# Performance work log

Hardware: AMD Instinct MI355X
Metric: run time of the kernel (lower is better)

Reference implementation:

```python
import jax, jax.numpy as jnp
import numpy as np

D_MODEL = 1024
NHEAD = 16
HEAD_DIM = D_MODEL // NHEAD


def setup_inputs() -> dict:
    key = jax.random.key(0)
    ks = jax.random.split(key, 9)
    s = 0.02
    x = jax.random.normal(ks[0], (2, 2048, D_MODEL), dtype=jnp.float32)
    Wq = jax.random.normal(ks[1], (D_MODEL, D_MODEL), dtype=jnp.float32) * s
    bq = jnp.zeros((D_MODEL,), jnp.float32)
    Wk = jax.random.normal(ks[2], (D_MODEL, D_MODEL), dtype=jnp.float32) * s
    bk = jnp.zeros((D_MODEL,), jnp.float32)
    Wv = jax.random.normal(ks[3], (D_MODEL, D_MODEL), dtype=jnp.float32) * s
    bv = jnp.zeros((D_MODEL,), jnp.float32)
    Wo = jax.random.normal(ks[4], (D_MODEL, D_MODEL), dtype=jnp.float32) * s
    bo = jnp.zeros((D_MODEL,), jnp.float32)
    return {"x": x, "Wq": Wq, "bq": bq, "Wk": Wk, "bk": bk,
            "Wv": Wv, "bv": bv, "Wo": Wo, "bo": bo}


def _rope(x, sin, cos):
    # x: [B, L, H, Dh]; rotate-half as in the torch module
    half = x.shape[-1] // 2
    x1, x2 = x[..., :half], x[..., half:]
    rotated = jnp.concatenate([-x2, x1], axis=-1)
    return x * cos + rotated * sin


def reference(x, Wq, bq, Wk, bk, Wv, bv, Wo, bo):
    B, L, D = x.shape
    H, Dh = NHEAD, HEAD_DIM
    q = (x @ Wq.T + bq).reshape(B, L, H, Dh)
    k = (x @ Wk.T + bk).reshape(B, L, H, Dh)
    v = (x @ Wv.T + bv).reshape(B, L, H, Dh)

    inv_freq = 1.0 / (10000.0 ** (jnp.arange(0, Dh, 2, dtype=jnp.float32) / Dh))
    t = jnp.arange(L, dtype=jnp.float32)
    freqs = jnp.einsum('i,j->ij', t, inv_freq)          # [L, Dh/2]
    emb = jnp.concatenate([freqs, freqs], axis=-1)      # [L, Dh]
    cos = jnp.cos(emb)[None, :, None, :]
    sin = jnp.sin(emb)[None, :, None, :]

    q = _rope(q, sin, cos)
    k = _rope(k, sin, cos)

    # [B, H, L, L]
    scores = jnp.einsum('bqhd,bkhd->bhqk', q, k) / jnp.sqrt(jnp.float32(Dh))
    attn = jax.nn.softmax(scores, axis=-1)
    # dropout in eval mode = identity (p given as 0.0)
    out = jnp.einsum('bhqk,bkhd->bqhd', attn, v).reshape(B, L, D)
    return out @ Wo.T + bo
```

## Files before the change

kernel.cpp:

```cpp
#include <hip/hip_runtime.h>
#include <math.h>

#define D_MODEL 1024
#define NHEAD 16
#define HEAD_DIM 64
#define L_SEQ 2048
#define BATCH 2
#define M_ROWS 4096
#define SC_Q 0.18033688011112042f

typedef __attribute__((ext_vector_type(8))) short short8;
typedef __attribute__((ext_vector_type(4))) float floatx4;
typedef __attribute__((ext_vector_type(2))) __fp16 half2_t;
typedef __attribute__((ext_vector_type(4))) __fp16 half4_t;
typedef __attribute__((ext_vector_type(8))) __fp16 half8_t;

#if __has_builtin(__builtin_amdgcn_exp2f)
#define EXP2F(x) __builtin_amdgcn_exp2f(x)
#else
#define EXP2F(x) exp2f(x)
#endif

__device__ inline unsigned f2bf_u(float x) {
    unsigned u = __float_as_uint(x);
    return (u + 0x7fffu + ((u >> 16) & 1u)) >> 16;
}

__device__ inline void gl_lds16(const void* g, void* l) {
    __builtin_amdgcn_global_load_lds((const __attribute__((address_space(1))) void*)g,
                                     (__attribute__((address_space(3))) void*)l, 16, 0, 0);
}

__device__ inline void permlane16_swap(unsigned& a, unsigned& b) {
#if __has_builtin(__builtin_amdgcn_permlane16_swap)
    auto r = __builtin_amdgcn_permlane16_swap(a, b, false, false);
    a = r[0];
    b = r[1];
#else
    asm("v_permlane16_swap_b32 %0, %1" : "+v"(a), "+v"(b));
#endif
}

__global__ __launch_bounds__(256) void cvt_all(
    const float* __restrict__ x,  const float* __restrict__ wq,
    const float* __restrict__ wk, const float* __restrict__ wv,
    const float* __restrict__ wo,
    unsigned short* __restrict__ xb,  unsigned short* __restrict__ wqb,
    unsigned short* __restrict__ wkb, unsigned short* __restrict__ wvb,
    unsigned short* __restrict__ wob, float* __restrict__ rt) {
    if (blockIdx.y == 5) {
        for (int idx = blockIdx.x * 256 + threadIdx.x; idx < L_SEQ * 16;
             idx += gridDim.x * 256) {
            int l = idx >> 4, f = idx & 15;
            float if0 = (float)pow(10000.0, -(double)f / 32.0);
            float if1 = (float)pow(10000.0, -(double)(f + 16) / 32.0);
            float s0, c0, s1, c1;
            sincosf((float)l * if0, &s0, &c0);
            sincosf((float)l * if1, &s1, &c1);
            float4 v = {c0, c1, s0, s1};
            *(float4*)(rt + (size_t)idx * 4) = v;
        }
        return;
    }
    const float* s; unsigned short* d; int n;
    switch (blockIdx.y) {
        case 0:  s = x;  d = xb;  n = M_ROWS * D_MODEL; break;
        case 1:  s = wq; d = wqb; n = D_MODEL * D_MODEL; break;
        case 2:  s = wk; d = wkb; n = D_MODEL * D_MODEL; break;
        case 3:  s = wv; d = wvb; n = D_MODEL * D_MODEL; break;
        default: s = wo; d = wob; n = D_MODEL * D_MODEL; break;
    }
    int stride = gridDim.x * 256 * 4;
    for (int i = (blockIdx.x * 256 + threadIdx.x) * 4; i < n; i += stride) {
        float4 v = *(const float4*)(s + i);
        ushort4 o;
        o.x = (unsigned short)f2bf_u(v.x);
        o.y = (unsigned short)f2bf_u(v.y);
        o.z = (unsigned short)f2bf_u(v.z);
        o.w = (unsigned short)f2bf_u(v.w);
        *(ushort4*)(d + i) = o;
    }
}

__global__ __launch_bounds__(256) void gemm_qkv(
    const unsigned short* __restrict__ xb,
    const unsigned short* __restrict__ wqb, const unsigned short* __restrict__ wkb,
    const unsigned short* __restrict__ wvb,
    const float* __restrict__ bq, const float* __restrict__ bk,
    const float* __restrict__ bv, const float* __restrict__ rt,
    unsigned short* __restrict__ qo, unsigned short* __restrict__ ko,
    unsigned short* __restrict__ vo) {
    __shared__ __align__(16) unsigned short As[128 * 32];
    __shared__ __align__(16) unsigned short Bs[128 * 32];

    const int K = D_MODEL;
    const int tid = threadIdx.x;
    const int lane = tid & 63;
    const int w = tid >> 6;
    const int wm = (w & 1) * 64;
    const int wn = (w >> 1) * 64;
    const int m0 = blockIdx.x * 128;
    const int n0 = blockIdx.y * 128;

    const unsigned short* Wsel; const float* bsel;
    unsigned short* osel; int mode; float oscale;
    if (blockIdx.z == 0)      { Wsel = wqb; bsel = bq; osel = qo; mode = 1; oscale = SC_Q; }
    else if (blockIdx.z == 1) { Wsel = wkb; bsel = bk; osel = ko; mode = 1; oscale = 1.0f; }
    else                      { Wsel = wvb; bsel = bv; osel = vo; mode = 2; oscale = 1.0f; }

    floatx4 acc[4][4];
#pragma unroll
    for (int i = 0; i < 4; ++i)
#pragma unroll
        for (int j = 0; j < 4; ++j) acc[i][j] = (floatx4){0.f, 0.f, 0.f, 0.f};

    const int sr = lane >> 2;
    const int ss = lane & 3;
    const unsigned short* Ag = xb + (size_t)m0 * K;
    const unsigned short* Bg = Wsel + (size_t)n0 * K;

    for (int k0 = 0; k0 < K; k0 += 32) {
        __syncthreads();
#pragma unroll
        for (int t = 0; t < 2; ++t) {
            int R0 = t * 64 + w * 16;
            int r = R0 + sr;
            int c = ss ^ ((r >> 1) & 3);
            gl_lds16(Ag + (size_t)r * K + k0 + c * 8, (void*)(As + R0 * 32));
            gl_lds16(Bg + (size_t)r * K + k0 + c * 8, (void*)(Bs + R0 * 32));
        }
        __syncthreads();

        short8 af[4], bf[4];
#pragma unroll
        for (int mt = 0; mt < 4; ++mt) {
            int ar = wm + mt * 16 + (lane & 15);
            int slot = (lane >> 4) ^ ((ar >> 1) & 3);
            af[mt] = *(const short8*)(As + ar * 32 + slot * 8);
        }
#pragma unroll
        for (int nt = 0; nt < 4; ++nt) {
            int br = wn + nt * 16 + (lane & 15);
            int slot = (lane >> 4) ^ ((br >> 1) & 3);
            bf[nt] = *(const short8*)(Bs + br * 32 + slot * 8);
        }
#pragma unroll
        for (int mt = 0; mt < 4; ++mt)
#pragma unroll
            for (int nt = 0; nt < 4; ++nt)
                acc[mt][nt] = __builtin_amdgcn_mfma_f32_16x16x32_bf16(
                    af[mt], bf[nt], acc[mt][nt], 0, 0, 0);
    }

#pragma unroll
    for (int nt = 0; nt < 4; ++nt) {
        float bn = bsel[n0 + wn + nt * 16 + (lane & 15)];
#pragma unroll
        for (int mt = 0; mt < 4; ++mt)
#pragma unroll
            for (int i = 0; i < 4; ++i) acc[mt][nt][i] += bn;
    }

    const int h = (n0 + wn) >> 6;

    if (mode == 1) {
#pragma unroll
        for (int mt = 0; mt < 4; ++mt)
#pragma unroll
            for (int i = 0; i < 4; ++i) {
                int m = m0 + wm + mt * 16 + (lane >> 4) * 4 + i;
                int b = m >> 11, l = m & (L_SEQ - 1);
                float4 tc = *(const float4*)(rt + ((size_t)(l * 16 + (lane & 15)) << 2));
#pragma unroll
                for (int nt = 0; nt < 4; ++nt) {
                    int dh = nt * 16 + (lane & 15);
                    float partner = acc[mt][nt ^ 2][i];
                    float rot = (nt < 2) ? -partner : partner;
                    float c = (nt & 1) ? tc.y : tc.x;
                    float s = (nt & 1) ? tc.w : tc.z;
                    float val = (acc[mt][nt][i] * c + rot * s) * oscale;
                    size_t idx = (((size_t)(b * NHEAD + h)) * L_SEQ + l) * HEAD_DIM + dh;
                    osel[idx] = (unsigned short)f2bf_u(val);
                }
            }
    } else {
#pragma unroll
        for (int mt = 0; mt < 4; ++mt)
#pragma unroll
            for (int ih = 0; ih < 4; ih += 2) {
                int m = m0 + wm + mt * 16 + (lane >> 4) * 4 + ih;
                int b = m >> 11, l = m & (L_SEQ - 1);
#pragma unroll
                for (int nt = 0; nt < 4; ++nt) {
                    int dh = nt * 16 + (lane & 15);
                    union { half2_t h; unsigned u; } cv;
                    cv.h = __builtin_amdgcn_cvt_pkrtz(acc[mt][nt][ih], acc[mt][nt][ih + 1]);
                    size_t idx = (((size_t)(b * NHEAD + h)) * HEAD_DIM + dh) * L_SEQ + l;
                    *(unsigned*)(vo + idx) = cv.u;
                }
            }
    }
}

__global__ __launch_bounds__(256) void gemm_out(
    const unsigned short* __restrict__ A, const unsigned short* __restrict__ Wb,
    const float* __restrict__ bias, float* __restrict__ out) {
    __shared__ __align__(16) unsigned short As[64 * 32];
    __shared__ __align__(16) unsigned short Bs[128 * 32];

    const int K = D_MODEL;
    const int tid = threadIdx.x;
    const int lane = tid & 63;
    const int w = tid >> 6;
    const int wm = (w & 1) * 32;
    const int wn = (w >> 1) * 64;
    const int m0 = blockIdx.x * 64;
    const int n0 = blockIdx.y * 128;

    floatx4 acc[2][4];
#pragma unroll
    for (int i = 0; i < 2; ++i)
#pragma unroll
        for (int j = 0; j < 4; ++j) acc[i][j] = (floatx4){0.f, 0.f, 0.f, 0.f};

    const int sr = lane >> 2;
    const int ss = lane & 3;
    const unsigned short* Ag = A + (size_t)m0 * K;
    const unsigned short* Bg = Wb + (size_t)n0 * K;

    for (int k0 = 0; k0 < K; k0 += 32) {
        __syncthreads();
        {
            int r = w * 16 + sr;
            int c = ss ^ ((r >> 1) & 3);
            gl_lds16(Ag + (size_t)r * K + k0 + c * 8, (void*)(As + (w * 16) * 32));
        }
#pragma unroll
        for (int t = 0; t < 2; ++t) {
            int R0 = t * 64 + w * 16;
            int r = R0 + sr;
            int c = ss ^ ((r >> 1) & 3);
            gl_lds16(Bg + (size_t)r * K + k0 + c * 8, (void*)(Bs + R0 * 32));
        }
        __syncthreads();

        short8 af[2], bf[4];
#pragma unroll
        for (int mt = 0; mt < 2; ++mt) {
            int ar = wm + mt * 16 + (lane & 15);
            int slot = (lane >> 4) ^ ((ar >> 1) & 3);
            af[mt] = *(const short8*)(As + ar * 32 + slot * 8);
        }
#pragma unroll
        for (int nt = 0; nt < 4; ++nt) {
            int br = wn + nt * 16 + (lane & 15);
            int slot = (lane >> 4) ^ ((br >> 1) & 3);
            bf[nt] = *(const short8*)(Bs + br * 32 + slot * 8);
        }
#pragma unroll
        for (int mt = 0; mt < 2; ++mt)
#pragma unroll
            for (int nt = 0; nt < 4; ++nt)
                acc[mt][nt] = __builtin_amdgcn_mfma_f32_16x16x32_bf16(
                    af[mt], bf[nt], acc[mt][nt], 0, 0, 0);
    }

#pragma unroll
    for (int nt = 0; nt < 4; ++nt) {
        int n = n0 + wn + nt * 16 + (lane & 15);
        float bn = bias[n];
#pragma unroll
        for (int mt = 0; mt < 2; ++mt)
#pragma unroll
            for (int i = 0; i < 4; ++i) {
                int m = m0 + wm + mt * 16 + (lane >> 4) * 4 + i;
                out[(size_t)m * D_MODEL + n] = acc[mt][nt][i] + bn;
            }
    }
}

template <int NZ>
__global__ __launch_bounds__(256, 4) void attn_mfma(
    const unsigned short* __restrict__ q, const unsigned short* __restrict__ k,
    const unsigned short* __restrict__ vt,
    float* __restrict__ opart, float* __restrict__ lpart,
    unsigned short* __restrict__ ao) {
    __shared__ __align__(16) unsigned short Ks[128 * 64];
    __shared__ __align__(16) unsigned short Vs[64 * 128];

    const int tid = threadIdx.x;
    const int lane = tid & 63;
    const int w = tid >> 6;
    const int quad = lane >> 4;
    const int ln = lane & 15;
    const int bh = blockIdx.y;
    const int q0 = blockIdx.x * 128;
    const int z = blockIdx.z;
    const int kvbase = z * (L_SEQ / NZ);

    const unsigned short* qb = q + (size_t)bh * L_SEQ * HEAD_DIM;
    const unsigned short* kb = k + (size_t)bh * L_SEQ * HEAD_DIM;
    const unsigned short* vb = vt + (size_t)bh * HEAD_DIM * L_SEQ;

    short8 qf[2][2];
#pragma unroll
    for (int ntq = 0; ntq < 2; ++ntq)
#pragma unroll
        for (int ks = 0; ks < 2; ++ks)
            qf[ntq][ks] = *(const short8*)(
                qb + (size_t)(q0 + w * 32 + ntq * 16 + ln) * HEAD_DIM
                + ks * 32 + quad * 8);

    floatx4 o[2][4];
    floatx4 ls[2];
#pragma unroll
    for (int ntq = 0; ntq < 2; ++ntq) {
        ls[ntq] = (floatx4){0.f, 0.f, 0.f, 0.f};
#pragma unroll
        for (int j = 0; j < 4; ++j) o[ntq][j] = (floatx4){0.f, 0.f, 0.f, 0.f};
    }

    half8_t ones8;
#pragma unroll
    for (int j = 0; j < 8; ++j) ones8[j] = (__fp16)1.0f;

    const int srk = lane >> 3;
    const int ssk = lane & 7;
    const int srv = lane >> 4;
    const int ssv = lane & 15;
    const int pb = ((quad & 1) << 1) | (quad >> 1);

    for (int t = 0; t < L_SEQ / (128 * NZ); ++t) {
        int kv0 = kvbase + t * 128;
        __syncthreads();
#pragma unroll
        for (int tt = 0; tt < 4; ++tt) {
            {
                int R0 = tt * 32 + w * 8;
                int r = R0 + srk;
                int c = ssk ^ (r & 7);
                gl_lds16(kb + (size_t)(kv0 + r) * HEAD_DIM + c * 8, (void*)(Ks + R0 * 64));
            }
            {
                int R0 = tt * 16 + w * 4;
                int r = R0 + srv;
                int c = ssv ^ (r & 15);
                gl_lds16(vb + (size_t)r * L_SEQ + kv0 + c * 8, (void*)(Vs + R0 * 128));
            }
        }
        __syncthreads();

#pragma unroll
        for (int mt2 = 0; mt2 < 4; ++mt2) {
            floatx4 s[2][2];
#pragma unroll
            for (int c = 0; c < 2; ++c) {
                int ar = mt2 * 32 + c * 16 + ln;
                short8 kf0 = *(const short8*)(Ks + ar * 64 + ((quad) ^ (ar & 7)) * 8);
                short8 kf1 = *(const short8*)(Ks + ar * 64 + ((4 + quad) ^ (ar & 7)) * 8);

                floatx4 t0 = (floatx4){0.f, 0.f, 0.f, 0.f};
                floatx4 t1 = (floatx4){0.f, 0.f, 0.f, 0.f};
                t0 = __builtin_amdgcn_mfma_f32_16x16x32_bf16(kf0, qf[0][0], t0, 0, 0, 0);
                t0 = __builtin_amdgcn_mfma_f32_16x16x32_bf16(kf1, qf[0][1], t0, 0, 0, 0);
                t1 = __builtin_amdgcn_mfma_f32_16x16x32_bf16(kf0, qf[1][0], t1, 0, 0, 0);
                t1 = __builtin_amdgcn_mfma_f32_16x16x32_bf16(kf1, qf[1][1], t1, 0, 0, 0);
                s[c][0] = t0;
                s[c][1] = t1;
            }

            half8_t vf[4];
#pragma unroll
            for (int ntd = 0; ntd < 4; ++ntd) {
                int row = ntd * 16 + ln;
                int slot = (mt2 * 4 + pb) ^ (row & 15);
                vf[ntd] = *(const half8_t*)(Vs + row * 128 + slot * 8);
            }

#pragma unroll
            for (int tq = 0; tq < 2; ++tq) {
                union { half2_t h; unsigned u; } c0l, c0h, c1l, c1h;
                c0l.h = __builtin_amdgcn_cvt_pkrtz(EXP2F(s[0][tq][0]), EXP2F(s[0][tq][1]));
                c0h.h = __builtin_amdgcn_cvt_pkrtz(EXP2F(s[0][tq][2]), EXP2F(s[0][tq][3]));
                c1l.h = __builtin_amdgcn_cvt_pkrtz(EXP2F(s[1][tq][0]), EXP2F(s[1][tq][1]));
                c1h.h = __builtin_amdgcn_cvt_pkrtz(EXP2F(s[1][tq][2]), EXP2F(s[1][tq][3]));
                unsigned a0 = c0l.u, b0 = c1l.u;
                unsigned a1 = c0h.u, b1 = c1h.u;
                permlane16_swap(a0, b0);
                permlane16_swap(a1, b1);
                union { half8_t h8; unsigned u[4]; } af;
                af.u[0] = a0; af.u[1] = a1; af.u[2] = b0; af.u[3] = b1;

                ls[tq] = __builtin_amdgcn_mfma_f32_16x16x32_f16(af.h8, ones8, ls[tq], 0, 0, 0);
#pragma unroll
                for (int ntd = 0; ntd < 4; ++ntd)
                    o[tq][ntd] = __builtin_amdgcn_mfma_f32_16x16x32_f16(
                        af.h8, vf[ntd], o[tq][ntd], 0, 0, 0);
            }
        }
    }

    if (NZ == 1) {
        const int b = bh >> 4, h = bh & (NHEAD - 1);
#pragma unroll
        for (int ntq = 0; ntq < 2; ++ntq)
#pragma unroll
            for (int i = 0; i < 4; ++i) {
                int l = q0 + w * 32 + ntq * 16 + quad * 4 + i;
                float inv = 1.0f / ls[ntq][i];
#pragma unroll
                for (int ntd = 0; ntd < 4; ++ntd) {
                    int dh = ntd * 16 + ln;
                    size_t idx = ((size_t)b * L_SEQ + l) * D_MODEL + h * HEAD_DIM + dh;
                    ao[idx] = (unsigned short)f2bf_u(o[ntq][ntd][i] * inv);
                }
            }
    } else {
        const size_t base = ((size_t)z * (BATCH * NHEAD) + bh) * L_SEQ;
#pragma unroll
        for (int ntq = 0; ntq < 2; ++ntq)
#pragma unroll
            for (int i = 0; i < 4; ++i) {
                int l = q0 + w * 32 + ntq * 16 + quad * 4 + i;
#pragma unroll
                for (int ntd = 0; ntd < 4; ++ntd) {
                    int dh = ntd * 16 + ln;
                    opart[(base + l) * HEAD_DIM + dh] = o[ntq][ntd][i];
                }
            }
        if (ln == 0) {
#pragma unroll
            for (int ntq = 0; ntq < 2; ++ntq)
#pragma unroll
                for (int i = 0; i < 4; ++i) {
                    int l = q0 + w * 32 + ntq * 16 + quad * 4 + i;
                    lpart[base + l] = ls[ntq][i];
                }
        }
    }
}

__global__ __launch_bounds__(256) void attn_combine(
    const float* __restrict__ opart, const float* __restrict__ lpart,
    unsigned short* __restrict__ ao) {
    const size_t R = (size_t)BATCH * NHEAD * L_SEQ;
    int e = blockIdx.x * 256 + threadIdx.x;
    int r = e >> 4;
    int dh0 = (e & 15) * 4;
    float4 a = *(const float4*)(opart + (size_t)r * HEAD_DIM + dh0);
    float4 c = *(const float4*)(opart + (R + r) * HEAD_DIM + dh0);
    float inv = 1.0f / (lpart[r] + lpart[R + r]);
    int bh = r >> 11, l = r & (L_SEQ - 1);
    int b = bh >> 4, h = bh & (NHEAD - 1);
    ushort4 ov;
    ov.x = (unsigned short)f2bf_u((a.x + c.x) * inv);
    ov.y = (unsigned short)f2bf_u((a.y + c.y) * inv);
    ov.z = (unsigned short)f2bf_u((a.z + c.z) * inv);
    ov.w = (unsigned short)f2bf_u((a.w + c.w) * inv);
    *(ushort4*)(ao + ((size_t)b * L_SEQ + l) * D_MODEL + h * HEAD_DIM + dh0) = ov;
}

extern "C" void kernel_launch(void* const* d_in, const int* in_sizes, int n_in,
                              void* d_out, int out_size, void* d_ws, size_t ws_size,
                              hipStream_t stream) {
    const float* x  = (const float*)d_in[0];
    const float* Wq = (const float*)d_in[1];
    const float* bq = (const float*)d_in[2];
    const float* Wk = (const float*)d_in[3];
    const float* bk = (const float*)d_in[4];
    const float* Wv = (const float*)d_in[5];
    const float* bv = (const float*)d_in[6];
    const float* Wo = (const float*)d_in[7];
    const float* bo = (const float*)d_in[8];
    float* outp = (float*)d_out;

    const size_t XE = (size_t)M_ROWS * D_MODEL;
    const size_t WE = (size_t)D_MODEL * D_MODEL;
    unsigned short* wqb = (unsigned short*)d_ws;
    unsigned short* wkb = wqb + WE;
    unsigned short* wvb = wkb + WE;
    unsigned short* wob = wvb + WE;
    unsigned short* qbf = wob + WE;
    unsigned short* kbf = qbf + XE;
    unsigned short* vtb = kbf + XE;
    unsigned short* xb  = vtb + XE;
    unsigned short* aob = xb;
    float* rt    = (float*)(xb + XE);
    float* lpart = rt;
    float* opart = rt + 131072;

    const size_t base_bytes  = (4 * WE + 4 * XE) * 2 + 131072 * 4;
    const size_t split_bytes = base_bytes + (size_t)8 * 1024 * 1024 * 4;
    const bool use_split = ws_size >= split_bytes;

    cvt_all<<<dim3(1024, 6), 256, 0, stream>>>(x, Wq, Wk, Wv, Wo,
                                               xb, wqb, wkb, wvb, wob, rt);

    gemm_qkv<<<dim3(M_ROWS / 128, D_MODEL / 128, 3), 256, 0, stream>>>(
        xb, wqb, wkb, wvb, bq, bk, bv, rt, qbf, kbf, vtb);

    if (use_split) {
        attn_mfma<2><<<dim3(L_SEQ / 128, BATCH * NHEAD, 2), 256, 0, stream>>>(
            qbf, kbf, vtb, opart, lpart, nullptr);
        attn_combine<<<dim3(4096), 256, 0, stream>>>(opart, lpart, aob);
    } else {
        attn_mfma<1><<<dim3(L_SEQ / 128, BATCH * NHEAD, 1), 256, 0, stream>>>(
            qbf, kbf, vtb, nullptr, nullptr, aob);
    }

    gemm_out<<<dim3(M_ROWS / 64, D_MODEL / 128), 256, 0, stream>>>(aob, wob, bo, outp);
}
```

Before: 197.5 us.

## Double-buffer K/V LDS tiles and remap workgroup order in attention kernel

Attention kernel now uses two LDS buffers for K and V tiles. It issues the next tile's global-to-LDS loads before computing on the current tile, so load latency overlaps with MFMA work and one barrier per iteration goes away. It also remaps the linear workgroup index with a stride-8 interleave, presumably to spread neighbouring blocks across XCDs for cache locality. LDS use doubles to 64KB per block, which may reduce occupancy under launch_bounds(256,4).

```diff
diff --git a/kernel.cpp b/kernel.cpp
--- a/kernel.cpp
+++ b/kernel.cpp
@@ -285,17 +285,23 @@
     const unsigned short* __restrict__ vt,
     float* __restrict__ opart, float* __restrict__ lpart,
     unsigned short* __restrict__ ao) {
-    __shared__ __align__(16) unsigned short Ks[128 * 64];
-    __shared__ __align__(16) unsigned short Vs[64 * 128];
+    __shared__ __align__(16) unsigned short Ks[2][128 * 64];
+    __shared__ __align__(16) unsigned short Vs[2][64 * 128];
 
     const int tid = threadIdx.x;
     const int lane = tid & 63;
     const int w = tid >> 6;
     const int quad = lane >> 4;
     const int ln = lane & 15;
-    const int bh = blockIdx.y;
-    const int q0 = blockIdx.x * 128;
-    const int z = blockIdx.z;
+
+    const int GX = L_SEQ / 128;
+    const int nwg = GX * BATCH * NHEAD * NZ;
+    int lin = (blockIdx.z * (BATCH * NHEAD) + blockIdx.y) * GX + blockIdx.x;
+    lin = (lin & 7) * (nwg >> 3) + (lin >> 3);
+    const int q0 = (lin & (GX - 1)) * 128;
+    const int rest = lin >> 4;
+    const int bh = rest & (BATCH * NHEAD - 1);
+    const int z = rest >> 5;
     const int kvbase = z * (L_SEQ / NZ);
 
     const unsigned short* qb = q + (size_t)bh * L_SEQ * HEAD_DIM;
@@ -330,34 +336,35 @@
     const int ssv = lane & 15;
     const int pb = ((quad & 1) << 1) | (quad >> 1);
 
-    for (int t = 0; t < L_SEQ / (128 * NZ); ++t) {
-        int kv0 = kvbase + t * 128;
-        __syncthreads();
+    auto stage_tile = [&](int buf, int kv0) {
 #pragma unroll
         for (int tt = 0; tt < 4; ++tt) {
             {
                 int R0 = tt * 32 + w * 8;
                 int r = R0 + srk;
                 int c = ssk ^ (r & 7);
-                gl_lds16(kb + (size_t)(kv0 + r) * HEAD_DIM + c * 8, (void*)(Ks + R0 * 64));
+                gl_lds16(kb + (size_t)(kv0 + r) * HEAD_DIM + c * 8,
+                         (void*)(Ks[buf] + R0 * 64));
             }
             {
                 int R0 = tt * 16 + w * 4;
                 int r = R0 + srv;
                 int c = ssv ^ (r & 15);
-                gl_lds16(vb + (size_t)r * L_SEQ + kv0 + c * 8, (void*)(Vs + R0 * 128));
-            }
-        }
-        __syncthreads();
-
+                gl_lds16(vb + (size_t)r * L_SEQ + kv0 + c * 8,
+                         (void*)(Vs[buf] + R0 * 128));
+            }
+        }
+    };
+
+    auto compute_tile = [&](const unsigned short* KsP, const unsigned short* VsP) {
 #pragma unroll
         for (int mt2 = 0; mt2 < 4; ++mt2) {
             floatx4 s[2][2];
 #pragma unroll
             for (int c = 0; c < 2; ++c) {
                 int ar = mt2 * 32 + c * 16 + ln;
-                short8 kf0 = *(const short8*)(Ks + ar * 64 + ((quad) ^ (ar & 7)) * 8);
-                short8 kf1 = *(const short8*)(Ks + ar * 64 + ((4 + quad) ^ (ar & 7)) * 8);
+                short8 kf0 = *(const short8*)(KsP + ar * 64 + ((quad) ^ (ar & 7)) * 8);
+                short8 kf1 = *(const short8*)(KsP + ar * 64 + ((4 + quad) ^ (ar & 7)) * 8);
 
                 floatx4 t0 = (floatx4){0.f, 0.f, 0.f, 0.f};
                 floatx4 t1 = (floatx4){0.f, 0.f, 0.f, 0.f};
@@ -374,7 +381,7 @@
             for (int ntd = 0; ntd < 4; ++ntd) {
                 int row = ntd * 16 + ln;
                 int slot = (mt2 * 4 + pb) ^ (row & 15);
-                vf[ntd] = *(const half8_t*)(Vs + row * 128 + slot * 8);
+                vf[ntd] = *(const half8_t*)(VsP + row * 128 + slot * 8);
             }
 
 #pragma unroll
@@ -397,6 +404,21 @@
                     o[tq][ntd] = __builtin_amdgcn_mfma_f32_16x16x32_f16(
                         af.h8, vf[ntd], o[tq][ntd], 0, 0, 0);
             }
+        }
+    };
+
+    const int NT = L_SEQ / (128 * NZ);
+    stage_tile(0, kvbase);
+    __syncthreads();
+    int cur = 0;
+    for (int t = 0; t < NT; ++t) {
+        if (t + 1 < NT) {
+            stage_tile(cur ^ 1, kvbase + (t + 1) * 128);
+            compute_tile(Ks[cur], Vs[cur]);
+            __syncthreads();
+            cur ^= 1;
+        } else {
+            compute_tile(Ks[cur], Vs[cur]);
         }
     }
 
```

After: 196.8 us. About the same (-0.4%).

## Drop split-KV attention and remap blocks so XCDs share heads

Applied to the files above, without the earlier changes.

Removes the two-way KV split and its combine kernel, so each attention block now processes the full sequence and writes normalized bf16 output directly. It also remaps the linear block index so that consecutive hardware-dispatched blocks (round-robin across the 8 XCDs) land on the same head's query tiles, improving K/V reuse in each XCD's L2. This removes the partial-output write/read traffic and one launch, but halves the grid to 512 blocks, which lowers parallelism and may leave CUs underused.

```diff
diff --git a/kernel.cpp b/kernel.cpp
--- a/kernel.cpp
+++ b/kernel.cpp
@@ -279,11 +279,9 @@
     }
 }
 
-template <int NZ>
 __global__ __launch_bounds__(256, 4) void attn_mfma(
     const unsigned short* __restrict__ q, const unsigned short* __restrict__ k,
     const unsigned short* __restrict__ vt,
-    float* __restrict__ opart, float* __restrict__ lpart,
     unsigned short* __restrict__ ao) {
     __shared__ __align__(16) unsigned short Ks[128 * 64];
     __shared__ __align__(16) unsigned short Vs[64 * 128];
@@ -293,10 +291,12 @@
     const int w = tid >> 6;
     const int quad = lane >> 4;
     const int ln = lane & 15;
-    const int bh = blockIdx.y;
-    const int q0 = blockIdx.x * 128;
-    const int z = blockIdx.z;
-    const int kvbase = z * (L_SEQ / NZ);
+
+    const int GX = L_SEQ / 128;
+    int lin = blockIdx.y * GX + blockIdx.x;
+    lin = (lin & 7) * 64 + (lin >> 3);
+    const int q0 = (lin & (GX - 1)) * 128;
+    const int bh = lin >> 4;
 
     const unsigned short* qb = q + (size_t)bh * L_SEQ * HEAD_DIM;
     const unsigned short* kb = k + (size_t)bh * L_SEQ * HEAD_DIM;
@@ -330,8 +330,8 @@
     const int ssv = lane & 15;
     const int pb = ((quad & 1) << 1) | (quad >> 1);
 
-    for (int t = 0; t < L_SEQ / (128 * NZ); ++t) {
-        int kv0 = kvbase + t * 128;
+    for (int t = 0; t < L_SEQ / 128; ++t) {
+        int kv0 = t * 128;
         __syncthreads();
 #pragma unroll
         for (int tt = 0; tt < 4; ++tt) {
@@ -400,64 +400,20 @@
         }
     }
 
-    if (NZ == 1) {
-        const int b = bh >> 4, h = bh & (NHEAD - 1);
-#pragma unroll
-        for (int ntq = 0; ntq < 2; ++ntq)
-#pragma unroll
-            for (int i = 0; i < 4; ++i) {
-                int l = q0 + w * 32 + ntq * 16 + quad * 4 + i;
-                float inv = 1.0f / ls[ntq][i];
-#pragma unroll
-                for (int ntd = 0; ntd < 4; ++ntd) {
-                    int dh = ntd * 16 + ln;
-                    size_t idx = ((size_t)b * L_SEQ + l) * D_MODEL + h * HEAD_DIM + dh;
-                    ao[idx] = (unsigned short)f2bf_u(o[ntq][ntd][i] * inv);
-                }
-            }
-    } else {
-        const size_t base = ((size_t)z * (BATCH * NHEAD) + bh) * L_SEQ;
-#pragma unroll
-        for (int ntq = 0; ntq < 2; ++ntq)
-#pragma unroll
-            for (int i = 0; i < 4; ++i) {
-                int l = q0 + w * 32 + ntq * 16 + quad * 4 + i;
-#pragma unroll
-                for (int ntd = 0; ntd < 4; ++ntd) {
-                    int dh = ntd * 16 + ln;
-                    opart[(base + l) * HEAD_DIM + dh] = o[ntq][ntd][i];
-                }
-            }
-        if (ln == 0) {
-#pragma unroll
-            for (int ntq = 0; ntq < 2; ++ntq)
-#pragma unroll
-                for (int i = 0; i < 4; ++i) {
-                    int l = q0 + w * 32 + ntq * 16 + quad * 4 + i;
-                    lpart[base + l] = ls[ntq][i];
-                }
-        }
-    }
-}
-
-__global__ __launch_bounds__(256) void attn_combine(
-    const float* __restrict__ opart, const float* __restrict__ lpart,
-    unsigned short* __restrict__ ao) {
-    const size_t R = (size_t)BATCH * NHEAD * L_SEQ;
-    int e = blockIdx.x * 256 + threadIdx.x;
-    int r = e >> 4;
-    int dh0 = (e & 15) * 4;
-    float4 a = *(const float4*)(opart + (size_t)r * HEAD_DIM + dh0);
-    float4 c = *(const float4*)(opart + (R + r) * HEAD_DIM + dh0);
-    float inv = 1.0f / (lpart[r] + lpart[R + r]);
-    int bh = r >> 11, l = r & (L_SEQ - 1);
-    int b = bh >> 4, h = bh & (NHEAD - 1);
-    ushort4 ov;
-    ov.x = (unsigned short)f2bf_u((a.x + c.x) * inv);
-    ov.y = (unsigned short)f2bf_u((a.y + c.y) * inv);
-    ov.z = (unsigned short)f2bf_u((a.z + c.z) * inv);
-    ov.w = (unsigned short)f2bf_u((a.w + c.w) * inv);
-    *(ushort4*)(ao + ((size_t)b * L_SEQ + l) * D_MODEL + h * HEAD_DIM + dh0) = ov;
+    const int b = bh >> 4, h = bh & (NHEAD - 1);
+#pragma unroll
+    for (int ntq = 0; ntq < 2; ++ntq)
+#pragma unroll
+        for (int i = 0; i < 4; ++i) {
+            int l = q0 + w * 32 + ntq * 16 + quad * 4 + i;
+            float inv = 1.0f / ls[ntq][i];
+#pragma unroll
+            for (int ntd = 0; ntd < 4; ++ntd) {
+                int dh = ntd * 16 + ln;
+                size_t idx = ((size_t)b * L_SEQ + l) * D_MODEL + h * HEAD_DIM + dh;
+                ao[idx] = (unsigned short)f2bf_u(o[ntq][ntd][i] * inv);
+            }
+        }
 }
 
 extern "C" void kernel_launch(void* const* d_in, const int* in_sizes, int n_in,
@@ -486,12 +442,6 @@
     unsigned short* xb  = vtb + XE;
     unsigned short* aob = xb;
     float* rt    = (float*)(xb + XE);
-    float* lpart = rt;
-    float* opart = rt + 131072;
-
-    const size_t base_bytes  = (4 * WE + 4 * XE) * 2 + 131072 * 4;
-    const size_t split_bytes = base_bytes + (size_t)8 * 1024 * 1024 * 4;
-    const bool use_split = ws_size >= split_bytes;
 
     cvt_all<<<dim3(1024, 6), 256, 0, stream>>>(x, Wq, Wk, Wv, Wo,
                                                xb, wqb, wkb, wvb, wob, rt);
@@ -499,14 +449,8 @@
     gemm_qkv<<<dim3(M_ROWS / 128, D_MODEL / 128, 3), 256, 0, stream>>>(
         xb, wqb, wkb, wvb, bq, bk, bv, rt, qbf, kbf, vtb);
 
-    if (use_split) {
-        attn_mfma<2><<<dim3(L_SEQ / 128, BATCH * NHEAD, 2), 256, 0, stream>>>(
-            qbf, kbf, vtb, opart, lpart, nullptr);
-        attn_combine<<<dim3(4096), 256, 0, stream>>>(opart, lpart, aob);
-    } else {
-        attn_mfma<1><<<dim3(L_SEQ / 128, BATCH * NHEAD, 1), 256, 0, stream>>>(
-            qbf, kbf, vtb, nullptr, nullptr, aob);
-    }
+    attn_mfma<<<dim3(L_SEQ / 128, BATCH * NHEAD), 256, 0, stream>>>(
+        qbf, kbf, vtb, aob);
 
     gemm_out<<<dim3(M_ROWS / 64, D_MODEL / 128), 256, 0, stream>>>(aob, wob, bo, outp);
 }
```

After: 188.9 us. -4.3%, faster.
